# Performance work log

Measured on AMD Instinct MI355X. Metric: run time of the kernel, lower is better.

The kernel has to match this reference:

```python
import jax, jax.numpy as jnp
import numpy as np

ALPHA = 0.9     # projection strength
EPS = 1e-3      # Lyapunov positive-definite regularizer (lyapunov_eps)
B, D, H = 32768, 512, 64


def setup_inputs() -> dict:
    key = jax.random.key(0)
    ks = jax.random.split(key, 8)
    def w(k, shape, fan_in):
        return jax.random.normal(k, shape, jnp.float32) * (1.0 / fan_in) ** 0.5
    return dict(
        x=jax.random.normal(ks[0], (B, D), jnp.float32),
        # dynamics MLP f(x): D -> 64 -> 64 -> D
        W1=w(ks[1], (D, H), D), b1=jnp.zeros((H,), jnp.float32),
        W2=w(ks[2], (H, H), H), b2=jnp.zeros((H,), jnp.float32),
        W3=w(ks[3], (H, D), H), b3=jnp.zeros((D,), jnp.float32),
        # Lyapunov MLP V(z): D -> 64 -> 64 -> 1 (+ eps*||z||^2)
        V1=w(ks[4], (D, H), D), c1=jnp.zeros((H,), jnp.float32),
        V2=w(ks[5], (H, H), H), c2=jnp.zeros((H,), jnp.float32),
        V3=w(ks[6], (H, 1), H), c3=jnp.zeros((1,), jnp.float32),
    )


def reference(x, W1, b1, W2, b2, W3, b3, V1, c1, V2, c2, V3, c3):
    def fnet(xx):  # nominal dynamics: [B,D] -> [B,D]
        h = jax.nn.relu(xx @ W1 + b1)
        h = jax.nn.relu(h @ W2 + b2)
        return h @ W3 + b3

    def vnet(z):  # Lyapunov candidate: [B,D] -> [B]
        h = jax.nn.relu(z @ V1 + c1)
        h = jax.nn.relu(h @ V2 + c2)
        return (h @ V3 + c3)[..., 0] + EPS * jnp.sum(z * z, axis=-1)

    def lyap_sum(xx):
        v = vnet(fnet(xx))
        return jnp.sum(v), v

    # grad_v replicates the in-forward lyapunov.backward(...): dV(f(x))/dx, shape [B,D]
    (_, lyap), grad_v = jax.value_and_grad(lyap_sum, has_aux=True)(x)

    f = fnet(x)                                   # [B, D]
    dot = jnp.sum(grad_v * grad_v, axis=-1)       # bmm(gv, fv): per-sample <grad_v, grad_v>
    denom = jnp.sum(grad_v * grad_v)              # global .pow(2).sum() over all elements
    orth = jax.nn.relu(dot + ALPHA * lyap) / denom  # [B]
    return f - orth[:, None] * grad_v             # diag_embed(orth) @ grad_v
```

## Files before the change

kernel.cpp:

```cpp
#include <hip/hip_runtime.h>

#define ALPHA_C 0.9f
#define EPS_C 1e-3f

typedef unsigned short u16;
typedef __attribute__((ext_vector_type(8))) short short8;
typedef __attribute__((ext_vector_type(4))) short short4v;
typedef __attribute__((ext_vector_type(4))) float f32x4;
#define MFMA(a, b, c) __builtin_amdgcn_mfma_f32_16x16x32_bf16(a, b, c, 0, 0, 0)
#define LDS_FENCE() asm volatile("" ::: "memory")
#define BAR_TOP()    { LDS_FENCE(); __builtin_amdgcn_s_barrier(); LDS_FENCE(); }
#define BAR_STAGED() { LDS_FENCE(); asm volatile("s_waitcnt lgkmcnt(0)" ::: "memory"); \
                       __builtin_amdgcn_s_barrier(); LDS_FENCE(); }

__device__ __forceinline__ u16 f2bf(float f) {
  union { float f; unsigned u; } v; v.f = f;
  unsigned u = v.u;
  u += 0x7FFFu + ((u >> 16) & 1u);
  return (u16)(u >> 16);
}
__device__ __forceinline__ float bf2f(u16 h) {
  union { unsigned u; float f; } v; v.u = ((unsigned)h) << 16;
  return v.f;
}

__global__ __launch_bounds__(256) void k_conv(
    const float* __restrict__ W1, const float* __restrict__ W2, const float* __restrict__ W3,
    const float* __restrict__ V1, const float* __restrict__ V2,
    u16* __restrict__ PW1T, u16* __restrict__ PW1n, u16* __restrict__ PV1T, u16* __restrict__ PV1n,
    u16* __restrict__ PW3T, u16* __restrict__ PW3n, u16* __restrict__ PW2T, u16* __restrict__ PW2n,
    u16* __restrict__ PV2T, u16* __restrict__ PV2n, float* __restrict__ DP) {
  int i = blockIdx.x * 256 + threadIdx.x;
  if (i < 256) DP[i] = 0.f;
  {
    int k = i >> 6, j = i & 63;
    u16 b = f2bf(W1[i]);
    PW1T[((((j >> 4) * 16 + (k >> 5)) * 4 + ((k & 31) >> 3)) * 16 + (j & 15)) * 8 + (k & 7)] = b;
    PW1n[((((k >> 4) * 2 + (j >> 5)) * 4 + ((j & 31) >> 3)) * 16 + (k & 15)) * 8 + (j & 7)] = b;
    u16 c = f2bf(V1[i]);
    PV1T[((((j >> 4) * 16 + (k >> 5)) * 4 + ((k & 31) >> 3)) * 16 + (j & 15)) * 8 + (k & 7)] = c;
    PV1n[((((k >> 4) * 2 + (j >> 5)) * 4 + ((j & 31) >> 3)) * 16 + (k & 15)) * 8 + (j & 7)] = c;
  }
  {
    int k = i >> 9, n = i & 511;
    u16 b = f2bf(W3[i]);
    PW3T[((((n >> 4) * 2 + (k >> 5)) * 4 + ((k & 31) >> 3)) * 16 + (n & 15)) * 8 + (k & 7)] = b;
    PW3n[((((k >> 4) * 16 + (n >> 5)) * 4 + ((n & 31) >> 3)) * 16 + (k & 15)) * 8 + (n & 7)] = b;
  }
  if (i < 4096) {
    int k = i >> 6, j = i & 63;
    u16 b = f2bf(W2[i]);
    PW2T[((((j >> 4) * 2 + (k >> 5)) * 4 + ((k & 31) >> 3)) * 16 + (j & 15)) * 8 + (k & 7)] = b;
    PW2n[((((k >> 4) * 2 + (j >> 5)) * 4 + ((j & 31) >> 3)) * 16 + (k & 15)) * 8 + (j & 7)] = b;
    u16 c = f2bf(V2[i]);
    PV2T[((((j >> 4) * 2 + (k >> 5)) * 4 + ((k & 31) >> 3)) * 16 + (j & 15)) * 8 + (k & 7)] = c;
    PV2n[((((k >> 4) * 2 + (j >> 5)) * 4 + ((j & 31) >> 3)) * 16 + (k & 15)) * 8 + (j & 7)] = c;
  }
}

#define LDG8(dst, P, FRAG)                                                      \
  _Pragma("unroll") for (int j = 0; j < 8; ++j)                                 \
    dst[j] = *(const short8*)&P[((size_t)(FRAG) * 64 + lane) * 8];

#define STAGE16(DST, P, SRCFRAG)                                                \
  _Pragma("unroll") for (int c = 0; c < 4; ++c)                                 \
    *(short8*)&Ws[((DST) * 512) + (c * 256 + tid) * 8] =                        \
      *(const short8*)&P[((size_t)(SRCFRAG) * 512) + (c * 256 + tid) * 8];

#define STAGE4x4(DST, P, OFF)                                                   \
  _Pragma("unroll") for (int t = 0; t < 4; ++t)                                 \
    *(short8*)&Ws[((DST) + t * 4) * 512 + tid * 8] =                            \
      *(const short8*)&P[((size_t)(t * 16 + (OFF))) * 512 + tid * 8];

__global__ __launch_bounds__(256, 2) void k_fused(
    const float* __restrict__ x,
    const u16* __restrict__ PW1T, const float* __restrict__ b1,
    const u16* __restrict__ PW2T, const float* __restrict__ b2,
    const u16* __restrict__ PW3T, const float* __restrict__ b3,
    const u16* __restrict__ PV1T, const float* __restrict__ c1,
    const u16* __restrict__ PV2T, const u16* __restrict__ PV2n, const float* __restrict__ c2,
    const float* __restrict__ V3, const float* __restrict__ c3,
    const u16* __restrict__ PV1n, const u16* __restrict__ PW3n,
    const u16* __restrict__ PW2n, const u16* __restrict__ PW1n,
    u16* __restrict__ FP, u16* __restrict__ T2P, u16* __restrict__ GVB,
    float* __restrict__ NUM, float* __restrict__ DP) {
  __shared__ __align__(16) u16 H1s[64 * 72];
  __shared__ __align__(16) u16 H2s[64 * 72];
  __shared__ __align__(16) u16 S2s[64 * 72];
  __shared__ __align__(16) u16 As[64 * 136];
  __shared__ __align__(16) u16 Ws[16384];
  __shared__ float dred[4];
  const int tid = threadIdx.x;
  const int lane = tid & 63, w = tid >> 6, q = lane >> 4, r = lane & 15;
  const int m0 = blockIdx.x * 64;
  const int arow = w * 16 + r;
  const int strip = blockIdx.x * 4 + w;
  const int h = lane >> 5, c4 = lane & 31;
  const float* xbase = x + (size_t)(m0 + w * 16) * 512;

  f32x4 acc1[4] = {};
  float4 xr[8];
  #pragma unroll
  for (int it = 0; it < 8; ++it)
    xr[it] = *(const float4*)&xbase[(it * 2 + h) * 512 + c4 * 4];
  #pragma unroll 1
  for (int kc = 0; kc < 4; ++kc) {
    BAR_TOP();
    STAGE4x4(0, PW1T, kc * 4);
    #pragma unroll
    for (int it = 0; it < 8; ++it) {
      float4 v = xr[it]; short4v s4;
      s4[0] = (short)f2bf(v.x); s4[1] = (short)f2bf(v.y);
      s4[2] = (short)f2bf(v.z); s4[3] = (short)f2bf(v.w);
      *(short4v*)&As[(w * 16 + it * 2 + h) * 136 + c4 * 4] = s4;
    }
    if (kc < 3) {
      #pragma unroll
      for (int it = 0; it < 8; ++it)
        xr[it] = *(const float4*)&xbase[(it * 2 + h) * 512 + (kc + 1) * 128 + c4 * 4];
    }
    BAR_STAGED();
    #pragma unroll
    for (int ks = 0; ks < 4; ++ks) {
      short8 a = *(const short8*)&As[arow * 136 + ks * 32 + q * 8];
      #pragma unroll
      for (int t = 0; t < 4; ++t) {
        short8 b = *(const short8*)&Ws[((t * 4 + ks) * 64 + lane) * 8];
        acc1[t] = MFMA(a, b, acc1[t]);
      }
    }
  }
  #pragma unroll
  for (int t = 0; t < 4; ++t) {
    int col = t * 16 + r; float bv = b1[col];
    #pragma unroll
    for (int g = 0; g < 4; ++g) {
      float hh = acc1[t][g] + bv; hh = hh > 0.f ? hh : 0.f;
      H1s[(w * 16 + q * 4 + g) * 72 + col] = f2bf(hh);
    }
  }
  LDS_FENCE();

  {
    short8 a0 = *(const short8*)&H1s[arow * 72 + 0 + q * 8];
    short8 a1 = *(const short8*)&H1s[arow * 72 + 32 + q * 8];
    f32x4 acc2[4] = {};
    #pragma unroll
    for (int t = 0; t < 4; ++t) {
      short8 b0 = *(const short8*)&PW2T[((t * 2 + 0) * 64 + lane) * 8];
      short8 b1 = *(const short8*)&PW2T[((t * 2 + 1) * 64 + lane) * 8];
      acc2[t] = MFMA(a0, b0, acc2[t]);
      acc2[t] = MFMA(a1, b1, acc2[t]);
    }
    #pragma unroll
    for (int t = 0; t < 4; ++t) {
      int col = t * 16 + r; float bv = b2[col];
      #pragma unroll
      for (int g = 0; g < 4; ++g) {
        float hh = acc2[t][g] + bv; hh = hh > 0.f ? hh : 0.f;
        H2s[(w * 16 + q * 4 + g) * 72 + col] = f2bf(hh);
      }
    }
  }
  LDS_FENCE();

  f32x4 g1acc[4] = {};
  float ssq[4] = {0.f, 0.f, 0.f, 0.f};
  short8 h2a0 = *(const short8*)&H2s[arow * 72 + 0 + q * 8];
  short8 h2a1 = *(const short8*)&H2s[arow * 72 + 32 + q * 8];
  #pragma unroll 1
  for (int nc = 0; nc < 4; ++nc) {
    BAR_TOP();
    STAGE16(0, PW3T, nc * 16);
    STAGE4x4(16, PV1T, nc * 4);
    BAR_STAGED();
    f32x4 facc[8] = {};
    #pragma unroll
    for (int t = 0; t < 8; ++t) {
      short8 b0 = *(const short8*)&Ws[((t * 2 + 0) * 64 + lane) * 8];
      short8 b1 = *(const short8*)&Ws[((t * 2 + 1) * 64 + lane) * 8];
      facc[t] = MFMA(h2a0, b0, facc[t]);
      facc[t] = MFMA(h2a1, b1, facc[t]);
    }
    #pragma unroll
    for (int t = 0; t < 8; ++t) {
      float bv = b3[nc * 128 + t * 16 + r];
      short4v s4;
      #pragma unroll
      for (int g = 0; g < 4; ++g) {
        float v = facc[t][g] + bv;
        ssq[g] += v * v;
        u16 bb = f2bf(v);
        As[(w * 16 + q * 4 + g) * 136 + t * 16 + r] = bb;
        s4[g] = (short)bb;
      }
      *(short4v*)&FP[(size_t)(((strip * 4 + nc) * 8 + t) * 64 + lane) * 4] = s4;
    }
    LDS_FENCE();
    #pragma unroll
    for (int ks = 0; ks < 4; ++ks) {
      short8 a = *(const short8*)&As[arow * 136 + ks * 32 + q * 8];
      #pragma unroll
      for (int t = 0; t < 4; ++t) {
        short8 b = *(const short8*)&Ws[((16 + t * 4 + ks) * 64 + lane) * 8];
        g1acc[t] = MFMA(a, b, g1acc[t]);
      }
    }
  }

  f32x4 g1v[4];
  #pragma unroll
  for (int t = 0; t < 4; ++t) {
    int col = t * 16 + r; float cv = c1[col];
    #pragma unroll
    for (int g = 0; g < 4; ++g) {
      float v = g1acc[t][g] + cv; v = v > 0.f ? v : 0.f;
      g1v[t][g] = v;
      S2s[(w * 16 + q * 4 + g) * 72 + col] = f2bf(v);
    }
  }
  LDS_FENCE();
  f32x4 g2acc[4] = {};
  {
    short8 a0 = *(const short8*)&S2s[arow * 72 + 0 + q * 8];
    short8 a1 = *(const short8*)&S2s[arow * 72 + 32 + q * 8];
    #pragma unroll
    for (int t = 0; t < 4; ++t) {
      short8 b0 = *(const short8*)&PV2T[((t * 2 + 0) * 64 + lane) * 8];
      short8 b1 = *(const short8*)&PV2T[((t * 2 + 1) * 64 + lane) * 8];
      g2acc[t] = MFMA(a0, b0, g2acc[t]);
      g2acc[t] = MFMA(a1, b1, g2acc[t]);
    }
  }
  float tot[4] = {0.f, 0.f, 0.f, 0.f};
  #pragma unroll
  for (int t = 0; t < 4; ++t) {
    int col = t * 16 + r;
    float c2v = c2[col], v3v = V3[col];
    #pragma unroll
    for (int g = 0; g < 4; ++g) {
      float pre = g2acc[t][g] + c2v;
      float g2 = pre > 0.f ? pre : 0.f;
      S2s[(w * 16 + q * 4 + g) * 72 + col] = pre > 0.f ? f2bf(v3v) : (u16)0;
      tot[g] += g2 * v3v;
    }
  }
  LDS_FENCE();
  f32x4 s2acc[4] = {};
  {
    short8 a0 = *(const short8*)&S2s[arow * 72 + 0 + q * 8];
    short8 a1 = *(const short8*)&S2s[arow * 72 + 32 + q * 8];
    #pragma unroll
    for (int t = 0; t < 4; ++t) {
      short8 b0 = *(const short8*)&PV2n[((t * 2 + 0) * 64 + lane) * 8];
      short8 b1 = *(const short8*)&PV2n[((t * 2 + 1) * 64 + lane) * 8];
      s2acc[t] = MFMA(a0, b0, s2acc[t]);
      s2acc[t] = MFMA(a1, b1, s2acc[t]);
    }
  }
  #pragma unroll
  for (int t = 0; t < 4; ++t) {
    int col = t * 16 + r;
    #pragma unroll
    for (int g = 0; g < 4; ++g) {
      float sv = g1v[t][g] > 0.f ? s2acc[t][g] : 0.f;
      S2s[(w * 16 + q * 4 + g) * 72 + col] = f2bf(sv);
    }
  }
  LDS_FENCE();
  float c3v = c3[0];
  float lyap_row[4];
  #pragma unroll
  for (int g = 0; g < 4; ++g) {
    float s = tot[g] + EPS_C * ssq[g];
    s += __shfl_xor(s, 1); s += __shfl_xor(s, 2); s += __shfl_xor(s, 4); s += __shfl_xor(s, 8);
    lyap_row[g] = s + c3v;
  }

  asm volatile("s_waitcnt vmcnt(0)" ::: "memory");

  f32x4 t3acc[4] = {};
  short8 s2a0 = *(const short8*)&S2s[arow * 72 + 0 + q * 8];
  short8 s2a1 = *(const short8*)&S2s[arow * 72 + 32 + q * 8];
  #pragma unroll 1
  for (int nc = 0; nc < 4; ++nc) {
    BAR_TOP();
    STAGE16(0, PV1n, nc * 16);
    STAGE4x4(16, PW3n, nc * 4);
    BAR_STAGED();
    short4v fpr[8];
    #pragma unroll
    for (int t = 0; t < 8; ++t)
      fpr[t] = *(const short4v*)&FP[(size_t)(((strip * 4 + nc) * 8 + t) * 64 + lane) * 4];
    f32x4 uacc[8] = {};
    #pragma unroll
    for (int t = 0; t < 8; ++t) {
      short8 b0 = *(const short8*)&Ws[((t * 2 + 0) * 64 + lane) * 8];
      short8 b1 = *(const short8*)&Ws[((t * 2 + 1) * 64 + lane) * 8];
      uacc[t] = MFMA(s2a0, b0, uacc[t]);
      uacc[t] = MFMA(s2a1, b1, uacc[t]);
    }
    #pragma unroll
    for (int t = 0; t < 8; ++t) {
      #pragma unroll
      for (int g = 0; g < 4; ++g) {
        As[(w * 16 + q * 4 + g) * 136 + t * 16 + r] =
            f2bf(uacc[t][g] + 2.f * EPS_C * bf2f((u16)fpr[t][g]));
      }
    }
    LDS_FENCE();
    #pragma unroll
    for (int ks = 0; ks < 4; ++ks) {
      short8 a = *(const short8*)&As[arow * 136 + ks * 32 + q * 8];
      #pragma unroll
      for (int t = 0; t < 4; ++t) {
        short8 b = *(const short8*)&Ws[((16 + t * 4 + ks) * 64 + lane) * 8];
        t3acc[t] = MFMA(a, b, t3acc[t]);
      }
    }
  }
  #pragma unroll
  for (int t = 0; t < 4; ++t) {
    int col = t * 16 + r;
    #pragma unroll
    for (int g = 0; g < 4; ++g) {
      int addr = (w * 16 + q * 4 + g) * 72 + col;
      u16 h2 = H2s[addr];
      H2s[addr] = h2 ? f2bf(t3acc[t][g]) : (u16)0;
    }
  }
  LDS_FENCE();
  f32x4 t2acc[4] = {};
  {
    short8 a0 = *(const short8*)&H2s[arow * 72 + 0 + q * 8];
    short8 a1 = *(const short8*)&H2s[arow * 72 + 32 + q * 8];
    #pragma unroll
    for (int t = 0; t < 4; ++t) {
      short8 b0 = *(const short8*)&PW2n[((t * 2 + 0) * 64 + lane) * 8];
      short8 b1 = *(const short8*)&PW2n[((t * 2 + 1) * 64 + lane) * 8];
      t2acc[t] = MFMA(a0, b0, t2acc[t]);
      t2acc[t] = MFMA(a1, b1, t2acc[t]);
    }
  }
  #pragma unroll
  for (int t = 0; t < 4; ++t) {
    int col = t * 16 + r;
    #pragma unroll
    for (int g = 0; g < 4; ++g) {
      int addr = (w * 16 + q * 4 + g) * 72 + col;
      u16 h1 = H1s[addr];
      H1s[addr] = h1 ? f2bf(t2acc[t][g]) : (u16)0;
    }
  }
  LDS_FENCE();
  short8 v0 = *(const short8*)&H1s[arow * 72 + 0 + q * 8];
  short8 v1 = *(const short8*)&H1s[arow * 72 + 32 + q * 8];
  *(short8*)&T2P[(size_t)((strip * 2 + 0) * 64 + lane) * 8] = v0;
  *(short8*)&T2P[(size_t)((strip * 2 + 1) * 64 + lane) * 8] = v1;
  float ssq2[4] = {0.f, 0.f, 0.f, 0.f};
  #pragma unroll 1
  for (int nc = 0; nc < 4; ++nc) {
    BAR_TOP();
    STAGE16(0, PW1n, nc * 16);
    BAR_STAGED();
    f32x4 acc[8] = {};
    #pragma unroll
    for (int t = 0; t < 8; ++t) {
      short8 b0 = *(const short8*)&Ws[((t * 2 + 0) * 64 + lane) * 8];
      short8 b1 = *(const short8*)&Ws[((t * 2 + 1) * 64 + lane) * 8];
      acc[t] = MFMA(v0, b0, acc[t]);
      acc[t] = MFMA(v1, b1, acc[t]);
    }
    if (GVB != nullptr) {
      #pragma unroll
      for (int t = 0; t < 8; ++t) {
        short4v s4;
        #pragma unroll
        for (int g = 0; g < 4; ++g) {
          float v = acc[t][g];
          ssq2[g] += v * v;
          s4[g] = (short)f2bf(v);
        }
        *(short4v*)&GVB[(size_t)(((strip * 4 + nc) * 8 + t) * 64 + lane) * 4] = s4;
      }
    } else {
      #pragma unroll
      for (int t = 0; t < 8; ++t)
        #pragma unroll
        for (int g = 0; g < 4; ++g) ssq2[g] += acc[t][g] * acc[t][g];
    }
  }
  float totw = 0.f;
  #pragma unroll
  for (int g = 0; g < 4; ++g) {
    float s = ssq2[g];
    s += __shfl_xor(s, 1); s += __shfl_xor(s, 2); s += __shfl_xor(s, 4); s += __shfl_xor(s, 8);
    if (r == 0) {
      int rowg = m0 + w * 16 + q * 4 + g;
      float nm = s + ALPHA_C * lyap_row[g];
      NUM[rowg] = nm > 0.f ? nm : 0.f;
    }
    s += __shfl_xor(s, 16); s += __shfl_xor(s, 32);
    totw += s;
  }
  if (lane == 0) dred[w] = totw;
  __syncthreads();
  if (tid == 0) atomicAdd(&DP[blockIdx.x & 255], dred[0] + dred[1] + dred[2] + dred[3]);
}

__global__ __launch_bounds__(256, 2) void k_out(
    const u16* __restrict__ T2P, const u16* __restrict__ PW1n,
    const u16* __restrict__ FP, const float* __restrict__ NUM, const float* __restrict__ DP,
    float* __restrict__ out) {
  __shared__ float red[256];
  __shared__ __align__(16) float OutS[64 * 132];
  const int tid = threadIdx.x;
  const int lane = tid & 63, w = tid >> 6, q = lane >> 4, r = lane & 15;
  const int m0 = blockIdx.x * 64;
  const int strip = blockIdx.x * 4 + w;
  red[tid] = DP[tid];
  __syncthreads();
  for (int s = 128; s >= 1; s >>= 1) {
    if (tid < s) red[tid] += red[tid + s];
    __syncthreads();
  }
  const float inv_denom = 1.f / red[0];
  float sc[4];
  #pragma unroll
  for (int g = 0; g < 4; ++g) sc[g] = NUM[m0 + w * 16 + q * 4 + g] * inv_denom;
  short8 a0 = *(const short8*)&T2P[(size_t)((strip * 2 + 0) * 64 + lane) * 8];
  short8 a1 = *(const short8*)&T2P[(size_t)((strip * 2 + 1) * 64 + lane) * 8];
  short8 bA[8], bB[8];
  LDG8(bA, PW1n, ((j >> 1) * 2 + (j & 1)));
  #pragma unroll 1
  for (int nc = 0; nc < 4; ++nc) {
    LDG8(bB, PW1n, ((nc * 8 + 4 + (j >> 1)) * 2 + (j & 1)));
    short4v fpr[8];
    #pragma unroll
    for (int t = 0; t < 8; ++t)
      fpr[t] = *(const short4v*)&FP[(size_t)(((strip * 4 + nc) * 8 + t) * 64 + lane) * 4];
    f32x4 acc[8] = {};
    #pragma unroll
    for (int t = 0; t < 4; ++t) {
      acc[t] = MFMA(a0, bA[t * 2 + 0], acc[t]);
      acc[t] = MFMA(a1, bA[t * 2 + 1], acc[t]);
    }
    int ncn = (nc + 1) & 3;
    LDG8(bA, PW1n, ((ncn * 8 + (j >> 1)) * 2 + (j & 1)));
    #pragma unroll
    for (int t = 0; t < 4; ++t) {
      acc[4 + t] = MFMA(a0, bB[t * 2 + 0], acc[4 + t]);
      acc[4 + t] = MFMA(a1, bB[t * 2 + 1], acc[4 + t]);
    }
    #pragma unroll
    for (int t = 0; t < 8; ++t) {
      #pragma unroll
      for (int g = 0; g < 4; ++g)
        OutS[(w * 16 + q * 4 + g) * 132 + t * 16 + r] =
            bf2f((u16)fpr[t][g]) - sc[g] * acc[t][g];
    }
    LDS_FENCE();
    #pragma unroll
    for (int jj = 0; jj < 8; ++jj) {
      f32x4 ov = *(const f32x4*)&OutS[(w * 16 + (lane >> 5) + jj * 2) * 132 + (lane & 31) * 4];
      *(f32x4*)&out[(size_t)(m0 + w * 16 + (lane >> 5) + jj * 2) * 512 + nc * 128 + (lane & 31) * 4] = ov;
    }
    LDS_FENCE();
  }
}

__global__ __launch_bounds__(256, 2) void k_out2(
    const u16* __restrict__ FP, const u16* __restrict__ GVB,
    const float* __restrict__ NUM, const float* __restrict__ DP,
    float* __restrict__ out) {
  __shared__ float red[256];
  __shared__ __align__(16) float OutS[64 * 132];
  const int tid = threadIdx.x;
  const int lane = tid & 63, w = tid >> 6, q = lane >> 4, r = lane & 15;
  const int m0 = blockIdx.x * 64;
  const int strip = blockIdx.x * 4 + w;
  const int h = lane >> 5, c4 = lane & 31;
  red[tid] = DP[tid];
  __syncthreads();
  for (int s = 128; s >= 1; s >>= 1) {
    if (tid < s) red[tid] += red[tid + s];
    __syncthreads();
  }
  const float inv_denom = 1.f / red[0];
  float sc[4];
  #pragma unroll
  for (int g = 0; g < 4; ++g) sc[g] = NUM[m0 + w * 16 + q * 4 + g] * inv_denom;
  #pragma unroll 1
  for (int nc = 0; nc < 4; ++nc) {
    #pragma unroll
    for (int t = 0; t < 8; ++t) {
      size_t base = (size_t)(((strip * 4 + nc) * 8 + t) * 64 + lane) * 4;
      short4v f4 = *(const short4v*)&FP[base];
      short4v g4 = *(const short4v*)&GVB[base];
      #pragma unroll
      for (int g = 0; g < 4; ++g)
        OutS[(w * 16 + q * 4 + g) * 132 + t * 16 + r] =
            bf2f((u16)f4[g]) - sc[g] * bf2f((u16)g4[g]);
    }
    LDS_FENCE();
    #pragma unroll
    for (int jj = 0; jj < 8; ++jj) {
      f32x4 ov = *(const f32x4*)&OutS[(w * 16 + h + jj * 2) * 132 + c4 * 4];
      *(f32x4*)&out[(size_t)(m0 + w * 16 + h + jj * 2) * 512 + nc * 128 + c4 * 4] = ov;
    }
    LDS_FENCE();
  }
}

extern "C" void kernel_launch(void* const* d_in, const int* in_sizes, int n_in,
                              void* d_out, int out_size, void* d_ws, size_t ws_size,
                              hipStream_t stream) {
  const float* x  = (const float*)d_in[0];
  const float* W1 = (const float*)d_in[1];
  const float* b1 = (const float*)d_in[2];
  const float* W2 = (const float*)d_in[3];
  const float* b2 = (const float*)d_in[4];
  const float* W3 = (const float*)d_in[5];
  const float* b3 = (const float*)d_in[6];
  const float* V1 = (const float*)d_in[7];
  const float* c1 = (const float*)d_in[8];
  const float* V2 = (const float*)d_in[9];
  const float* c2 = (const float*)d_in[10];
  const float* V3 = (const float*)d_in[11];
  const float* c3 = (const float*)d_in[12];
  float* out = (float*)d_out;

  u16* FP  = (u16*)d_ws;
  u16* T2P = FP + 16777216;
  float* NUM = (float*)(T2P + 2097152);
  float* DP  = NUM + 32768;
  u16* PW1T = (u16*)(DP + 256);
  u16* PW1n = PW1T + 32768;
  u16* PV1T = PW1n + 32768;
  u16* PV1n = PV1T + 32768;
  u16* PW3T = PV1n + 32768;
  u16* PW3n = PW3T + 32768;
  u16* PW2T = PW3n + 32768;
  u16* PW2n = PW2T + 4096;
  u16* PV2T = PW2n + 4096;
  u16* PV2n = PV2T + 4096;
  u16* GVB_base = PV2n + 4096;
  size_t need_bytes = ((size_t)(GVB_base - (u16*)d_ws) + 16777216) * sizeof(u16);
  u16* GVB = (ws_size >= need_bytes) ? GVB_base : nullptr;

  k_conv<<<128, 256, 0, stream>>>(W1, W2, W3, V1, V2,
                                  PW1T, PW1n, PV1T, PV1n, PW3T, PW3n,
                                  PW2T, PW2n, PV2T, PV2n, DP);
  k_fused<<<512, 256, 0, stream>>>(x, PW1T, b1, PW2T, b2, PW3T, b3, PV1T, c1,
                                   PV2T, PV2n, c2, V3, c3, PV1n, PW3n, PW2n, PW1n,
                                   FP, T2P, GVB, NUM, DP);
  if (GVB != nullptr) {
    k_out2<<<512, 256, 0, stream>>>(FP, GVB, NUM, DP, out);
  } else {
    k_out<<<512, 256, 0, stream>>>(T2P, PW1n, FP, NUM, DP, out);
  }
}
```

Before: 180.3 us.

## Split fused kernel N-dimension across two wave halves with 512-thread blocks

Doubles the block to 512 threads (8 waves), so each 16-row strip is now handled by two waves that each compute half of the output columns in every GEMM stage. Per-row reductions (Lyapunov value and gradient norm) are combined across the two halves through LDS. Local fences become full block barriers, since each wave now reads H1/H2/S2/As tiles written by its partner. The aim is more waves per CU and fewer accumulator registers per wave to hide latency, at the price of extra barriers and staging split over more threads.

```diff
diff --git a/kernel.cpp b/kernel.cpp
--- a/kernel.cpp
+++ b/kernel.cpp
@@ -62,17 +62,19 @@
   _Pragma("unroll") for (int j = 0; j < 8; ++j)                                 \
     dst[j] = *(const short8*)&P[((size_t)(FRAG) * 64 + lane) * 8];
 
-#define STAGE16(DST, P, SRCFRAG)                                                \
-  _Pragma("unroll") for (int c = 0; c < 4; ++c)                                 \
-    *(short8*)&Ws[((DST) * 512) + (c * 256 + tid) * 8] =                        \
-      *(const short8*)&P[((size_t)(SRCFRAG) * 512) + (c * 256 + tid) * 8];
-
-#define STAGE4x4(DST, P, OFF)                                                   \
-  _Pragma("unroll") for (int t = 0; t < 4; ++t)                                 \
-    *(short8*)&Ws[((DST) + t * 4) * 512 + tid * 8] =                            \
-      *(const short8*)&P[((size_t)(t * 16 + (OFF))) * 512 + tid * 8];
-
-__global__ __launch_bounds__(256, 2) void k_fused(
+#define STAGE16B(DST, P, SRCFRAG)                                               \
+  _Pragma("unroll") for (int c = 0; c < 2; ++c)                                 \
+    *(short8*)&Ws[((DST) * 512) + (c * 512 + tid) * 8] =                        \
+      *(const short8*)&P[((size_t)(SRCFRAG) * 512) + (c * 512 + tid) * 8];
+
+#define STAGE4x4B(DST, P, OFF)                                                  \
+  _Pragma("unroll") for (int c = 0; c < 2; ++c) {                               \
+    int t_ = c * 2 + (tid >> 8);                                                \
+    *(short8*)&Ws[((DST) + t_ * 4) * 512 + (tid & 255) * 8] =                   \
+      *(const short8*)&P[((size_t)(t_ * 16 + (OFF))) * 512 + (tid & 255) * 8];  \
+  }
+
+__global__ __launch_bounds__(512, 4) void k_fused(
     const float* __restrict__ x,
     const u16* __restrict__ PW1T, const float* __restrict__ b1,
     const u16* __restrict__ PW2T, const float* __restrict__ b2,
@@ -92,318 +94,334 @@
   __shared__ float dred[4];
   const int tid = threadIdx.x;
   const int lane = tid & 63, w = tid >> 6, q = lane >> 4, r = lane & 15;
+  const int ws = w & 3, wh = w >> 2;
   const int m0 = blockIdx.x * 64;
-  const int arow = w * 16 + r;
-  const int strip = blockIdx.x * 4 + w;
-  const int h = lane >> 5, c4 = lane & 31;
-  const float* xbase = x + (size_t)(m0 + w * 16) * 512;
-
-  f32x4 acc1[4] = {};
-  float4 xr[8];
-  #pragma unroll
-  for (int it = 0; it < 8; ++it)
-    xr[it] = *(const float4*)&xbase[(it * 2 + h) * 512 + c4 * 4];
-  #pragma unroll 1
-  for (int kc = 0; kc < 4; ++kc) {
-    BAR_TOP();
-    STAGE4x4(0, PW1T, kc * 4);
-    #pragma unroll
-    for (int it = 0; it < 8; ++it) {
-      float4 v = xr[it]; short4v s4;
-      s4[0] = (short)f2bf(v.x); s4[1] = (short)f2bf(v.y);
-      s4[2] = (short)f2bf(v.z); s4[3] = (short)f2bf(v.w);
-      *(short4v*)&As[(w * 16 + it * 2 + h) * 136 + c4 * 4] = s4;
-    }
-    if (kc < 3) {
-      #pragma unroll
-      for (int it = 0; it < 8; ++it)
-        xr[it] = *(const float4*)&xbase[(it * 2 + h) * 512 + (kc + 1) * 128 + c4 * 4];
-    }
-    BAR_STAGED();
-    #pragma unroll
-    for (int ks = 0; ks < 4; ++ks) {
-      short8 a = *(const short8*)&As[arow * 136 + ks * 32 + q * 8];
-      #pragma unroll
-      for (int t = 0; t < 4; ++t) {
-        short8 b = *(const short8*)&Ws[((t * 4 + ks) * 64 + lane) * 8];
-        acc1[t] = MFMA(a, b, acc1[t]);
-      }
-    }
-  }
-  #pragma unroll
-  for (int t = 0; t < 4; ++t) {
-    int col = t * 16 + r; float bv = b1[col];
+  const int arow = ws * 16 + r;
+  const int strip = blockIdx.x * 4 + ws;
+  float* xf = (float*)As;
+
+  f32x4 acc1[2] = {};
+  {
+    const int L = (wh << 6) | lane, h4 = L >> 5, cc = L & 31;
+    const float* xb = x + (size_t)(m0 + ws * 16) * 512;
+    float4 xr[4];
+    #pragma unroll
+    for (int it = 0; it < 4; ++it)
+      xr[it] = *(const float4*)&xb[(it * 4 + h4) * 512 + cc * 4];
+    #pragma unroll 1
+    for (int kc = 0; kc < 4; ++kc) {
+      BAR_TOP();
+      STAGE4x4B(0, PW1T, kc * 4);
+      #pragma unroll
+      for (int it = 0; it < 4; ++it) {
+        float4 v = xr[it]; short4v s4;
+        s4[0] = (short)f2bf(v.x); s4[1] = (short)f2bf(v.y);
+        s4[2] = (short)f2bf(v.z); s4[3] = (short)f2bf(v.w);
+        *(short4v*)&As[(ws * 16 + it * 4 + h4) * 136 + cc * 4] = s4;
+      }
+      if (kc < 3) {
+        #pragma unroll
+        for (int it = 0; it < 4; ++it)
+          xr[it] = *(const float4*)&xb[(it * 4 + h4) * 512 + (kc + 1) * 128 + cc * 4];
+      }
+      BAR_STAGED();
+      #pragma unroll
+      for (int ks = 0; ks < 4; ++ks) {
+        short8 a = *(const short8*)&As[arow * 136 + ks * 32 + q * 8];
+        #pragma unroll
+        for (int tt = 0; tt < 2; ++tt) {
+          short8 b = *(const short8*)&Ws[(((wh * 2 + tt) * 4 + ks) * 64 + lane) * 8];
+          acc1[tt] = MFMA(a, b, acc1[tt]);
+        }
+      }
+    }
+  }
+  #pragma unroll
+  for (int tt = 0; tt < 2; ++tt) {
+    int col = (wh * 2 + tt) * 16 + r; float bv = b1[col];
     #pragma unroll
     for (int g = 0; g < 4; ++g) {
-      float hh = acc1[t][g] + bv; hh = hh > 0.f ? hh : 0.f;
-      H1s[(w * 16 + q * 4 + g) * 72 + col] = f2bf(hh);
-    }
-  }
-  LDS_FENCE();
+      float hh = acc1[tt][g] + bv; hh = hh > 0.f ? hh : 0.f;
+      H1s[(ws * 16 + q * 4 + g) * 72 + col] = f2bf(hh);
+    }
+  }
+  BAR_STAGED();
 
   {
     short8 a0 = *(const short8*)&H1s[arow * 72 + 0 + q * 8];
     short8 a1 = *(const short8*)&H1s[arow * 72 + 32 + q * 8];
-    f32x4 acc2[4] = {};
-    #pragma unroll
-    for (int t = 0; t < 4; ++t) {
+    f32x4 acc2[2] = {};
+    #pragma unroll
+    for (int tt = 0; tt < 2; ++tt) {
+      int t = wh * 2 + tt;
       short8 b0 = *(const short8*)&PW2T[((t * 2 + 0) * 64 + lane) * 8];
       short8 b1 = *(const short8*)&PW2T[((t * 2 + 1) * 64 + lane) * 8];
-      acc2[t] = MFMA(a0, b0, acc2[t]);
-      acc2[t] = MFMA(a1, b1, acc2[t]);
-    }
-    #pragma unroll
-    for (int t = 0; t < 4; ++t) {
-      int col = t * 16 + r; float bv = b2[col];
+      acc2[tt] = MFMA(a0, b0, acc2[tt]);
+      acc2[tt] = MFMA(a1, b1, acc2[tt]);
+    }
+    #pragma unroll
+    for (int tt = 0; tt < 2; ++tt) {
+      int col = (wh * 2 + tt) * 16 + r; float bv = b2[col];
       #pragma unroll
       for (int g = 0; g < 4; ++g) {
-        float hh = acc2[t][g] + bv; hh = hh > 0.f ? hh : 0.f;
-        H2s[(w * 16 + q * 4 + g) * 72 + col] = f2bf(hh);
-      }
-    }
-  }
-  LDS_FENCE();
-
-  f32x4 g1acc[4] = {};
-  float ssq[4] = {0.f, 0.f, 0.f, 0.f};
+        float hh = acc2[tt][g] + bv; hh = hh > 0.f ? hh : 0.f;
+        H2s[(ws * 16 + q * 4 + g) * 72 + col] = f2bf(hh);
+      }
+    }
+  }
+  BAR_STAGED();
   short8 h2a0 = *(const short8*)&H2s[arow * 72 + 0 + q * 8];
   short8 h2a1 = *(const short8*)&H2s[arow * 72 + 32 + q * 8];
+
+  f32x4 g1acc[2] = {};
+  float ssqp[4] = {0.f, 0.f, 0.f, 0.f};
   #pragma unroll 1
   for (int nc = 0; nc < 4; ++nc) {
     BAR_TOP();
-    STAGE16(0, PW3T, nc * 16);
-    STAGE4x4(16, PV1T, nc * 4);
+    STAGE16B(0, PW3T, nc * 16);
+    STAGE4x4B(16, PV1T, nc * 4);
     BAR_STAGED();
-    f32x4 facc[8] = {};
-    #pragma unroll
-    for (int t = 0; t < 8; ++t) {
+    f32x4 facc[4] = {};
+    #pragma unroll
+    for (int tt = 0; tt < 4; ++tt) {
+      int t = wh * 4 + tt;
       short8 b0 = *(const short8*)&Ws[((t * 2 + 0) * 64 + lane) * 8];
       short8 b1 = *(const short8*)&Ws[((t * 2 + 1) * 64 + lane) * 8];
-      facc[t] = MFMA(h2a0, b0, facc[t]);
-      facc[t] = MFMA(h2a1, b1, facc[t]);
-    }
-    #pragma unroll
-    for (int t = 0; t < 8; ++t) {
+      facc[tt] = MFMA(h2a0, b0, facc[tt]);
+      facc[tt] = MFMA(h2a1, b1, facc[tt]);
+    }
+    #pragma unroll
+    for (int tt = 0; tt < 4; ++tt) {
+      int t = wh * 4 + tt;
       float bv = b3[nc * 128 + t * 16 + r];
       short4v s4;
       #pragma unroll
       for (int g = 0; g < 4; ++g) {
-        float v = facc[t][g] + bv;
-        ssq[g] += v * v;
+        float v = facc[tt][g] + bv;
+        ssqp[g] += v * v;
         u16 bb = f2bf(v);
-        As[(w * 16 + q * 4 + g) * 136 + t * 16 + r] = bb;
+        As[(ws * 16 + q * 4 + g) * 136 + t * 16 + r] = bb;
         s4[g] = (short)bb;
       }
       *(short4v*)&FP[(size_t)(((strip * 4 + nc) * 8 + t) * 64 + lane) * 4] = s4;
     }
-    LDS_FENCE();
+    BAR_STAGED();
     #pragma unroll
     for (int ks = 0; ks < 4; ++ks) {
       short8 a = *(const short8*)&As[arow * 136 + ks * 32 + q * 8];
       #pragma unroll
-      for (int t = 0; t < 4; ++t) {
+      for (int tt = 0; tt < 2; ++tt) {
+        int t = wh * 2 + tt;
         short8 b = *(const short8*)&Ws[((16 + t * 4 + ks) * 64 + lane) * 8];
-        g1acc[t] = MFMA(a, b, g1acc[t]);
-      }
-    }
-  }
-
-  f32x4 g1v[4];
-  #pragma unroll
-  for (int t = 0; t < 4; ++t) {
-    int col = t * 16 + r; float cv = c1[col];
+        g1acc[tt] = MFMA(a, b, g1acc[tt]);
+      }
+    }
+  }
+
+  f32x4 g1v[2];
+  #pragma unroll
+  for (int tt = 0; tt < 2; ++tt) {
+    int col = (wh * 2 + tt) * 16 + r; float cv = c1[col];
     #pragma unroll
     for (int g = 0; g < 4; ++g) {
-      float v = g1acc[t][g] + cv; v = v > 0.f ? v : 0.f;
-      g1v[t][g] = v;
-      S2s[(w * 16 + q * 4 + g) * 72 + col] = f2bf(v);
-    }
-  }
-  LDS_FENCE();
-  f32x4 g2acc[4] = {};
+      float v = g1acc[tt][g] + cv; v = v > 0.f ? v : 0.f;
+      g1v[tt][g] = v;
+      S2s[(ws * 16 + q * 4 + g) * 72 + col] = f2bf(v);
+    }
+  }
+  BAR_STAGED();
+  f32x4 g2acc[2] = {};
   {
     short8 a0 = *(const short8*)&S2s[arow * 72 + 0 + q * 8];
     short8 a1 = *(const short8*)&S2s[arow * 72 + 32 + q * 8];
     #pragma unroll
-    for (int t = 0; t < 4; ++t) {
+    for (int tt = 0; tt < 2; ++tt) {
+      int t = wh * 2 + tt;
       short8 b0 = *(const short8*)&PV2T[((t * 2 + 0) * 64 + lane) * 8];
       short8 b1 = *(const short8*)&PV2T[((t * 2 + 1) * 64 + lane) * 8];
-      g2acc[t] = MFMA(a0, b0, g2acc[t]);
-      g2acc[t] = MFMA(a1, b1, g2acc[t]);
-    }
-  }
-  float tot[4] = {0.f, 0.f, 0.f, 0.f};
-  #pragma unroll
-  for (int t = 0; t < 4; ++t) {
-    int col = t * 16 + r;
+      g2acc[tt] = MFMA(a0, b0, g2acc[tt]);
+      g2acc[tt] = MFMA(a1, b1, g2acc[tt]);
+    }
+  }
+  float totp[4] = {0.f, 0.f, 0.f, 0.f};
+  #pragma unroll
+  for (int tt = 0; tt < 2; ++tt) {
+    int col = (wh * 2 + tt) * 16 + r;
     float c2v = c2[col], v3v = V3[col];
     #pragma unroll
     for (int g = 0; g < 4; ++g) {
-      float pre = g2acc[t][g] + c2v;
+      float pre = g2acc[tt][g] + c2v;
       float g2 = pre > 0.f ? pre : 0.f;
-      S2s[(w * 16 + q * 4 + g) * 72 + col] = pre > 0.f ? f2bf(v3v) : (u16)0;
-      tot[g] += g2 * v3v;
-    }
-  }
-  LDS_FENCE();
-  f32x4 s2acc[4] = {};
+      S2s[(ws * 16 + q * 4 + g) * 72 + col] = pre > 0.f ? f2bf(v3v) : (u16)0;
+      totp[g] += g2 * v3v;
+    }
+  }
+  BAR_STAGED();
+  f32x4 s2acc[2] = {};
   {
     short8 a0 = *(const short8*)&S2s[arow * 72 + 0 + q * 8];
     short8 a1 = *(const short8*)&S2s[arow * 72 + 32 + q * 8];
     #pragma unroll
-    for (int t = 0; t < 4; ++t) {
+    for (int tt = 0; tt < 2; ++tt) {
+      int t = wh * 2 + tt;
       short8 b0 = *(const short8*)&PV2n[((t * 2 + 0) * 64 + lane) * 8];
       short8 b1 = *(const short8*)&PV2n[((t * 2 + 1) * 64 + lane) * 8];
-      s2acc[t] = MFMA(a0, b0, s2acc[t]);
-      s2acc[t] = MFMA(a1, b1, s2acc[t]);
-    }
-  }
-  #pragma unroll
-  for (int t = 0; t < 4; ++t) {
-    int col = t * 16 + r;
+      s2acc[tt] = MFMA(a0, b0, s2acc[tt]);
+      s2acc[tt] = MFMA(a1, b1, s2acc[tt]);
+    }
+  }
+  #pragma unroll
+  for (int tt = 0; tt < 2; ++tt) {
+    int col = (wh * 2 + tt) * 16 + r;
     #pragma unroll
     for (int g = 0; g < 4; ++g) {
-      float sv = g1v[t][g] > 0.f ? s2acc[t][g] : 0.f;
-      S2s[(w * 16 + q * 4 + g) * 72 + col] = f2bf(sv);
-    }
-  }
-  LDS_FENCE();
+      float sv = g1v[tt][g] > 0.f ? s2acc[tt][g] : 0.f;
+      S2s[(ws * 16 + q * 4 + g) * 72 + col] = f2bf(sv);
+    }
+  }
+  BAR_STAGED();
+  #pragma unroll
+  for (int g = 0; g < 4; ++g) {
+    float s = totp[g] + EPS_C * ssqp[g];
+    s += __shfl_xor(s, 1); s += __shfl_xor(s, 2); s += __shfl_xor(s, 4); s += __shfl_xor(s, 8);
+    if (r == 0) xf[w * 16 + q * 4 + g] = s;
+  }
+  BAR_STAGED();
   float c3v = c3[0];
   float lyap_row[4];
   #pragma unroll
-  for (int g = 0; g < 4; ++g) {
-    float s = tot[g] + EPS_C * ssq[g];
-    s += __shfl_xor(s, 1); s += __shfl_xor(s, 2); s += __shfl_xor(s, 4); s += __shfl_xor(s, 8);
-    lyap_row[g] = s + c3v;
-  }
+  for (int g = 0; g < 4; ++g)
+    lyap_row[g] = xf[w * 16 + q * 4 + g] + xf[(w ^ 4) * 16 + q * 4 + g] + c3v;
 
   asm volatile("s_waitcnt vmcnt(0)" ::: "memory");
 
-  f32x4 t3acc[4] = {};
+  f32x4 t3acc[2] = {};
   short8 s2a0 = *(const short8*)&S2s[arow * 72 + 0 + q * 8];
   short8 s2a1 = *(const short8*)&S2s[arow * 72 + 32 + q * 8];
   #pragma unroll 1
   for (int nc = 0; nc < 4; ++nc) {
     BAR_TOP();
-    STAGE16(0, PV1n, nc * 16);
-    STAGE4x4(16, PW3n, nc * 4);
+    STAGE16B(0, PV1n, nc * 16);
+    STAGE4x4B(16, PW3n, nc * 4);
     BAR_STAGED();
-    short4v fpr[8];
-    #pragma unroll
-    for (int t = 0; t < 8; ++t)
-      fpr[t] = *(const short4v*)&FP[(size_t)(((strip * 4 + nc) * 8 + t) * 64 + lane) * 4];
-    f32x4 uacc[8] = {};
-    #pragma unroll
-    for (int t = 0; t < 8; ++t) {
+    short4v fpr[4];
+    #pragma unroll
+    for (int tt = 0; tt < 4; ++tt)
+      fpr[tt] = *(const short4v*)&FP[(size_t)(((strip * 4 + nc) * 8 + wh * 4 + tt) * 64 + lane) * 4];
+    f32x4 uacc[4] = {};
+    #pragma unroll
+    for (int tt = 0; tt < 4; ++tt) {
+      int t = wh * 4 + tt;
       short8 b0 = *(const short8*)&Ws[((t * 2 + 0) * 64 + lane) * 8];
       short8 b1 = *(const short8*)&Ws[((t * 2 + 1) * 64 + lane) * 8];
-      uacc[t] = MFMA(s2a0, b0, uacc[t]);
-      uacc[t] = MFMA(s2a1, b1, uacc[t]);
-    }
-    #pragma unroll
-    for (int t = 0; t < 8; ++t) {
+      uacc[tt] = MFMA(s2a0, b0, uacc[tt]);
+      uacc[tt] = MFMA(s2a1, b1, uacc[tt]);
+    }
+    #pragma unroll
+    for (int tt = 0; tt < 4; ++tt) {
+      int t = wh * 4 + tt;
       #pragma unroll
       for (int g = 0; g < 4; ++g) {
-        As[(w * 16 + q * 4 + g) * 136 + t * 16 + r] =
-            f2bf(uacc[t][g] + 2.f * EPS_C * bf2f((u16)fpr[t][g]));
-      }
-    }
-    LDS_FENCE();
+        As[(ws * 16 + q * 4 + g) * 136 + t * 16 + r] =
+            f2bf(uacc[tt][g] + 2.f * EPS_C * bf2f((u16)fpr[tt][g]));
+      }
+    }
+    BAR_STAGED();
     #pragma unroll
     for (int ks = 0; ks < 4; ++ks) {
       short8 a = *(const short8*)&As[arow * 136 + ks * 32 + q * 8];
       #pragma unroll
-      for (int t = 0; t < 4; ++t) {
+      for (int tt = 0; tt < 2; ++tt) {
+        int t = wh * 2 + tt;
         short8 b = *(const short8*)&Ws[((16 + t * 4 + ks) * 64 + lane) * 8];
-        t3acc[t] = MFMA(a, b, t3acc[t]);
-      }
-    }
-  }
-  #pragma unroll
-  for (int t = 0; t < 4; ++t) {
-    int col = t * 16 + r;
+        t3acc[tt] = MFMA(a, b, t3acc[tt]);
+      }
+    }
+  }
+  #pragma unroll
+  for (int tt = 0; tt < 2; ++tt) {
+    int col = (wh * 2 + tt) * 16 + r;
     #pragma unroll
     for (int g = 0; g < 4; ++g) {
-      int addr = (w * 16 + q * 4 + g) * 72 + col;
+      int addr = (ws * 16 + q * 4 + g) * 72 + col;
       u16 h2 = H2s[addr];
-      H2s[addr] = h2 ? f2bf(t3acc[t][g]) : (u16)0;
-    }
-  }
-  LDS_FENCE();
-  f32x4 t2acc[4] = {};
+      H2s[addr] = h2 ? f2bf(t3acc[tt][g]) : (u16)0;
+    }
+  }
+  BAR_STAGED();
+  f32x4 t2acc[2] = {};
   {
     short8 a0 = *(const short8*)&H2s[arow * 72 + 0 + q * 8];
     short8 a1 = *(const short8*)&H2s[arow * 72 + 32 + q * 8];
     #pragma unroll
-    for (int t = 0; t < 4; ++t) {
+    for (int tt = 0; tt < 2; ++tt) {
+      int t = wh * 2 + tt;
       short8 b0 = *(const short8*)&PW2n[((t * 2 + 0) * 64 + lane) * 8];
       short8 b1 = *(const short8*)&PW2n[((t * 2 + 1) * 64 + lane) * 8];
-      t2acc[t] = MFMA(a0, b0, t2acc[t]);
-      t2acc[t] = MFMA(a1, b1, t2acc[t]);
-    }
-  }
-  #pragma unroll
-  for (int t = 0; t < 4; ++t) {
-    int col = t * 16 + r;
+      t2acc[tt] = MFMA(a0, b0, t2acc[tt]);
+      t2acc[tt] = MFMA(a1, b1, t2acc[tt]);
+    }
+  }
+  #pragma unroll
+  for (int tt = 0; tt < 2; ++tt) {
+    int col = (wh * 2 + tt) * 16 + r;
     #pragma unroll
     for (int g = 0; g < 4; ++g) {
-      int addr = (w * 16 + q * 4 + g) * 72 + col;
+      int addr = (ws * 16 + q * 4 + g) * 72 + col;
       u16 h1 = H1s[addr];
-      H1s[addr] = h1 ? f2bf(t2acc[t][g]) : (u16)0;
-    }
-  }
-  LDS_FENCE();
+      H1s[addr] = h1 ? f2bf(t2acc[tt][g]) : (u16)0;
+    }
+  }
+  BAR_STAGED();
   short8 v0 = *(const short8*)&H1s[arow * 72 + 0 + q * 8];
   short8 v1 = *(const short8*)&H1s[arow * 72 + 32 + q * 8];
-  *(short8*)&T2P[(size_t)((strip * 2 + 0) * 64 + lane) * 8] = v0;
-  *(short8*)&T2P[(size_t)((strip * 2 + 1) * 64 + lane) * 8] = v1;
-  float ssq2[4] = {0.f, 0.f, 0.f, 0.f};
+  if (wh == 0) *(short8*)&T2P[(size_t)((strip * 2 + 0) * 64 + lane) * 8] = v0;
+  else         *(short8*)&T2P[(size_t)((strip * 2 + 1) * 64 + lane) * 8] = v1;
+
+  float ssq2p[4] = {0.f, 0.f, 0.f, 0.f};
   #pragma unroll 1
   for (int nc = 0; nc < 4; ++nc) {
     BAR_TOP();
-    STAGE16(0, PW1n, nc * 16);
+    STAGE16B(0, PW1n, nc * 16);
     BAR_STAGED();
-    f32x4 acc[8] = {};
-    #pragma unroll
-    for (int t = 0; t < 8; ++t) {
+    #pragma unroll
+    for (int tt = 0; tt < 4; ++tt) {
+      int t = wh * 4 + tt;
       short8 b0 = *(const short8*)&Ws[((t * 2 + 0) * 64 + lane) * 8];
       short8 b1 = *(const short8*)&Ws[((t * 2 + 1) * 64 + lane) * 8];
-      acc[t] = MFMA(v0, b0, acc[t]);
-      acc[t] = MFMA(v1, b1, acc[t]);
-    }
-    if (GVB != nullptr) {
-      #pragma unroll
-      for (int t = 0; t < 8; ++t) {
-        short4v s4;
-        #pragma unroll
-        for (int g = 0; g < 4; ++g) {
-          float v = acc[t][g];
-          ssq2[g] += v * v;
-          s4[g] = (short)f2bf(v);
-        }
+      f32x4 a = {};
+      a = MFMA(v0, b0, a);
+      a = MFMA(v1, b1, a);
+      short4v s4;
+      #pragma unroll
+      for (int g = 0; g < 4; ++g) {
+        ssq2p[g] += a[g] * a[g];
+        s4[g] = (short)f2bf(a[g]);
+      }
+      if (GVB != nullptr)
         *(short4v*)&GVB[(size_t)(((strip * 4 + nc) * 8 + t) * 64 + lane) * 4] = s4;
-      }
-    } else {
-      #pragma unroll
-      for (int t = 0; t < 8; ++t)
-        #pragma unroll
-        for (int g = 0; g < 4; ++g) ssq2[g] += acc[t][g] * acc[t][g];
-    }
-  }
+    }
+  }
+  #pragma unroll
+  for (int g = 0; g < 4; ++g) {
+    float s = ssq2p[g];
+    s += __shfl_xor(s, 1); s += __shfl_xor(s, 2); s += __shfl_xor(s, 4); s += __shfl_xor(s, 8);
+    if (r == 0) xf[w * 16 + q * 4 + g] = s;
+  }
+  BAR_STAGED();
   float totw = 0.f;
   #pragma unroll
   for (int g = 0; g < 4; ++g) {
-    float s = ssq2[g];
-    s += __shfl_xor(s, 1); s += __shfl_xor(s, 2); s += __shfl_xor(s, 4); s += __shfl_xor(s, 8);
-    if (r == 0) {
-      int rowg = m0 + w * 16 + q * 4 + g;
+    float s = xf[w * 16 + q * 4 + g] + xf[(w ^ 4) * 16 + q * 4 + g];
+    if (r == 0 && wh == 0) {
+      int rowg = m0 + ws * 16 + q * 4 + g;
       float nm = s + ALPHA_C * lyap_row[g];
       NUM[rowg] = nm > 0.f ? nm : 0.f;
     }
     s += __shfl_xor(s, 16); s += __shfl_xor(s, 32);
     totw += s;
   }
-  if (lane == 0) dred[w] = totw;
+  if (lane == 0 && wh == 0) dred[ws] = totw;
   __syncthreads();
   if (tid == 0) atomicAdd(&DP[blockIdx.x & 255], dred[0] + dred[1] + dred[2] + dred[3]);
 }
@@ -551,7 +569,7 @@
   k_conv<<<128, 256, 0, stream>>>(W1, W2, W3, V1, V2,
                                   PW1T, PW1n, PV1T, PV1n, PW3T, PW3n,
                                   PW2T, PW2n, PV2T, PV2n, DP);
-  k_fused<<<512, 256, 0, stream>>>(x, PW1T, b1, PW2T, b2, PW3T, b3, PV1T, c1,
+  k_fused<<<512, 512, 0, stream>>>(x, PW1T, b1, PW2T, b2, PW3T, b3, PV1T, c1,
                                    PV2T, PV2n, c2, V3, c3, PV1n, PW3n, PW2n, PW1n,
                                    FP, T2P, GVB, NUM, DP);
   if (GVB != nullptr) {
```

Measured after the change: 175.2 us. 2.9% less time.
